# Kernel optimization log

Measured on AMD Instinct MI355X. Metric: run time of the kernel, lower is better.

## Reference

```python
import jax, jax.numpy as jnp
import numpy as np

N, E, G = 100000, 1600000, 64   # nodes, edges, graphs
IN, H, OUT = 32, 128, 3


def setup_inputs() -> dict:
    key = jax.random.key(0)
    ks = jax.random.split(key, 24)
    def w(k, i, o):
        return (jax.random.normal(k, (i, o), jnp.float32) / np.sqrt(i)).astype(jnp.float32)
    inp = {
        "x": jax.random.normal(ks[0], (N, IN), jnp.float32),
        "edge_index": jax.random.randint(ks[1], (2, E), 0, N, dtype=jnp.int32).astype(jnp.int64),
        "batch": jnp.sort(jax.random.randint(ks[2], (N,), 0, G, dtype=jnp.int32)).astype(jnp.int64),
        # SAGEConv layer 0 (in->hidden): lin_l (neighbors, with bias), lin_r (root, no bias)
        "Wl0": w(ks[3], IN, H), "bl0": jnp.zeros((H,), jnp.float32), "Wr0": w(ks[4], IN, H),
        # SAGEConv layers 1,2 (hidden->hidden)
        "Wl1": w(ks[5], H, H), "bl1": jnp.zeros((H,), jnp.float32), "Wr1": w(ks[6], H, H),
        "Wl2": w(ks[7], H, H), "bl2": jnp.zeros((H,), jnp.float32), "Wr2": w(ks[8], H, H),
        # output head
        "Wfc": w(ks[9], H, OUT), "bfc": jnp.zeros((OUT,), jnp.float32),
        # aux MLP on (dim1, dim3)
        "Wa1": w(ks[10], 2, H), "ba1": jnp.zeros((H,), jnp.float32),
        "Wa2": w(ks[11], H, H), "ba2": jnp.zeros((H,), jnp.float32),
        "Wao": w(ks[12], H, 1), "bao": jnp.zeros((1,), jnp.float32),
    }
    return inp


def _sage_conv(x, src, dst, Wl, bl, Wr):
    # PyG SAGEConv (mean aggr): out = lin_l(mean_{j in N(i)} x_j) + lin_r(x_i)
    msg = x[src]                                   # [E, d] gather
    agg = jax.ops.segment_sum(msg, dst, num_segments=N)
    cnt = jax.ops.segment_sum(jnp.ones((src.shape[0],), x.dtype), dst, num_segments=N)
    mean = agg / jnp.maximum(cnt, 1.0)[:, None]
    return mean @ Wl + bl + x @ Wr


def reference(x, edge_index, batch,
              Wl0, bl0, Wr0, Wl1, bl1, Wr1, Wl2, bl2, Wr2,
              Wfc, bfc, Wa1, ba1, Wa2, ba2, Wao, bao):
    src, dst = edge_index[0], edge_index[1]
    h = jax.nn.relu(_sage_conv(x, src, dst, Wl0, bl0, Wr0))   # dropout is identity in eval
    h = jax.nn.relu(_sage_conv(h, src, dst, Wl1, bl1, Wr1))
    h = jax.nn.relu(_sage_conv(h, src, dst, Wl2, bl2, Wr2))
    main = h @ Wfc + bfc                                      # [N, 3]
    dim1, dim3 = main[:, 0], main[:, 2]
    aux_in = jnp.stack([dim1, dim3], axis=-1)                 # [N, 2]
    a = jax.nn.relu(aux_in @ Wa1 + ba1)
    a = jax.nn.relu(a @ Wa2 + ba2)
    aux_out = (a @ Wao + bao)[:, 0]                           # [N]
    final = jnp.stack([dim1, aux_out, dim3], axis=-1)         # [N, 3]
    # global mean pool over graph ids
    s = jax.ops.segment_sum(final, batch, num_segments=G)
    c = jax.ops.segment_sum(jnp.ones((final.shape[0],), final.dtype), batch, num_segments=G)
    return s / jnp.maximum(c, 1.0)[:, None]                   # [G, 3]
```

## Files before the change

### kernel.cpp

```cpp
#include <hip/hip_runtime.h>

#define NR 128
#define PART_CH 4096
typedef unsigned short ushortT;
typedef __attribute__((ext_vector_type(8))) short short8;
typedef __attribute__((ext_vector_type(4))) float float4v;
typedef __attribute__((ext_vector_type(2))) float float2v;

__device__ __forceinline__ unsigned short f32_to_bf16_rne(float f) {
    unsigned u = __float_as_uint(f);
    unsigned r = (u + 0x7fffu + ((u >> 16) & 1u)) >> 16;
    return (unsigned short)r;
}

__device__ __forceinline__ unsigned char f32_to_fp8(float f) {
    return (unsigned char)(__builtin_amdgcn_cvt_pk_fp8_f32(f, f, 0, false) & 0xff);
}

__device__ __forceinline__ void accum8(float* acc, uint4 v) {
    unsigned u[4] = {v.x, v.y, v.z, v.w};
#pragma unroll
    for (int q = 0; q < 4; q++) {
        acc[2 * q]     += __uint_as_float(u[q] << 16);
        acc[2 * q + 1] += __uint_as_float(u[q] & 0xffff0000u);
    }
}

__device__ __forceinline__ void accum16_fp8(float* acc, uint4 v) {
    unsigned u[4] = {v.x, v.y, v.z, v.w};
#pragma unroll
    for (int q = 0; q < 4; q++) {
        float2v lo = __builtin_amdgcn_cvt_pk_f32_fp8(u[q], false);
        float2v hi = __builtin_amdgcn_cvt_pk_f32_fp8(u[q], true);
        acc[4 * q + 0] += lo.x;
        acc[4 * q + 1] += lo.y;
        acc[4 * q + 2] += hi.x;
        acc[4 * q + 3] += hi.y;
    }
}


__launch_bounds__(256)
__global__ void bucket_count(const int* __restrict__ dst, int* __restrict__ bcnt, int E, int NB) {
    __shared__ int h[1024];
    int t = threadIdx.x;
    for (int j = t; j < NB; j += 256) h[j] = 0;
    __syncthreads();
    int e0 = blockIdx.x * PART_CH;
    int e1 = min(e0 + PART_CH, E);
    for (int base = e0; base < e1; base += 2048) {
        int idx = base + t;
        int d[8];
        int cnt = 0;
#pragma unroll
        for (int u = 0; u < 8; u++) {
            int e = idx + u * 256;
            if (e < e1) d[cnt++] = dst[e];
        }
        for (int u = 0; u < cnt; u++) atomicAdd(&h[d[u] >> 7], 1);
    }
    __syncthreads();
    for (int j = t; j < NB; j += 256) {
        int v = h[j];
        if (v) atomicAdd(&bcnt[j], v);
    }
}

__launch_bounds__(256)
__global__ void bucket_scan(const int* __restrict__ bcnt, int* __restrict__ bstart,
                            int* __restrict__ gcur, int NB, int E) {
    __shared__ int sh[256];
    int t = threadIdx.x;
    int v[4];
    int tot = 0;
#pragma unroll
    for (int j = 0; j < 4; j++) {
        int idx = t * 4 + j;
        v[j] = (idx < NB) ? bcnt[idx] : 0;
        tot += v[j];
    }
    sh[t] = tot;
    __syncthreads();
    for (int off = 1; off < 256; off <<= 1) {
        int add = (t >= off) ? sh[t - off] : 0;
        __syncthreads();
        sh[t] += add;
        __syncthreads();
    }
    int run = sh[t] - tot;
#pragma unroll
    for (int j = 0; j < 4; j++) {
        int idx = t * 4 + j;
        if (idx < NB) { bstart[idx] = run; gcur[idx] = run; }
        run += v[j];
    }
    if (t == 0) bstart[NB] = E;
}

__launch_bounds__(256)
__global__ void partition_edges(const int* __restrict__ src, const int* __restrict__ dst,
                                int* __restrict__ gcur, unsigned* __restrict__ packed,
                                int E, int NB) {
    __shared__ int hist[1024];
    __shared__ int base[1024];
    int t = threadIdx.x;
    int e0 = blockIdx.x * PART_CH;
    int e1 = min(e0 + PART_CH, E);
    for (int j = t; j < NB; j += 256) hist[j] = 0;
    __syncthreads();
    for (int bb = e0; bb < e1; bb += 2048) {
        int idx = bb + t;
        int d[8];
        int cnt = 0;
#pragma unroll
        for (int u = 0; u < 8; u++) {
            int e = idx + u * 256;
            if (e < e1) d[cnt++] = dst[e];
        }
        for (int u = 0; u < cnt; u++) atomicAdd(&hist[d[u] >> 7], 1);
    }
    __syncthreads();
    for (int j = t; j < NB; j += 256) {
        int h = hist[j];
        base[j] = h ? atomicAdd(&gcur[j], h) : 0;
    }
    __syncthreads();
    for (int j = t; j < NB; j += 256) hist[j] = base[j];
    __syncthreads();
    for (int bb = e0; bb < e1; bb += 2048) {
        int idx = bb + t;
        int d[8], s[8];
        int cnt = 0;
#pragma unroll
        for (int u = 0; u < 8; u++) {
            int e = idx + u * 256;
            if (e < e1) { d[cnt] = dst[e]; s[cnt] = src[e]; cnt++; }
        }
        for (int u = 0; u < cnt; u++) {
            int dd = d[u];
            int pos = atomicAdd(&hist[dd >> 7], 1);
            packed[pos] = (unsigned)s[u] | ((unsigned)(dd & (NR - 1)) << 17);
        }
    }
}

__launch_bounds__(256)
__global__ void bucket_sort(const unsigned* __restrict__ packed, const int* __restrict__ bstart,
                            int* __restrict__ row_start, int* __restrict__ srcs, int N) {
    __shared__ int cnt[NR];
    __shared__ int sc[NR];
    __shared__ int cur[NR];
    int b = blockIdx.x, t = threadIdx.x;
    int nb0 = b * NR;
    int nnode = min(NR, N - nb0);
    int lo = bstart[b], hi = bstart[b + 1];
    if (t < NR) cnt[t] = 0;
    __syncthreads();
    for (int bb = lo; bb < hi; bb += 2048) {
        int idx = bb + t;
        unsigned pk[8];
        int c = 0;
#pragma unroll
        for (int u = 0; u < 8; u++) {
            int e = idx + u * 256;
            if (e < hi) pk[c++] = packed[e];
        }
        for (int u = 0; u < c; u++) atomicAdd(&cnt[pk[u] >> 17], 1);
    }
    __syncthreads();
    if (t < NR) sc[t] = cnt[t];
    __syncthreads();
    for (int off = 1; off < NR; off <<= 1) {
        int add = (t >= off && t < NR) ? sc[t - off] : 0;
        __syncthreads();
        if (t < NR) sc[t] += add;
        __syncthreads();
    }
    if (t < nnode) {
        int s = lo + sc[t] - cnt[t];
        row_start[nb0 + t] = s;
        cur[t] = s;
    }
    if (t == 0 && nb0 + nnode == N) row_start[N] = hi;
    __syncthreads();
    for (int bb = lo; bb < hi; bb += 2048) {
        int idx = bb + t;
        unsigned pk[8];
        int c = 0;
#pragma unroll
        for (int u = 0; u < 8; u++) {
            int e = idx + u * 256;
            if (e < hi) pk[c++] = packed[e];
        }
        for (int u = 0; u < c; u++) {
            int pos = atomicAdd(&cur[pk[u] >> 17], 1);
            srcs[pos] = (int)(pk[u] & 0x1FFFFu);
        }
    }
}


__global__ void prep_fused(const float* __restrict__ x, ushortT* __restrict__ xbf, int n4,
                           const float* __restrict__ Wl0, const float* __restrict__ Wr0,
                           const float* __restrict__ Wl1, const float* __restrict__ Wr1,
                           const float* __restrict__ Wl2, const float* __restrict__ Wr2,
                           const float* __restrict__ Wa2,
                           ushortT* __restrict__ Wt0, ushortT* __restrict__ Wt1,
                           ushortT* __restrict__ Wt2, ushortT* __restrict__ Wa2t) {
    int tid0 = blockIdx.x * 256 + threadIdx.x;
    if (tid0 < n4) {
        float4 v = ((const float4*)x)[tid0];
        ushort4 o;
        o.x = f32_to_bf16_rne(v.x);
        o.y = f32_to_bf16_rne(v.y);
        o.z = f32_to_bf16_rne(v.z);
        o.w = f32_to_bf16_rne(v.w);
        ((ushort4*)xbf)[tid0] = o;
        return;
    }
    int tid = tid0 - n4;
    if (tid < 8192) {
        int col = tid >> 6, k = tid & 63;
        float v = (k < 32) ? Wl0[k * 128 + col] : Wr0[(k - 32) * 128 + col];
        Wt0[col * 64 + ((k + 8 * col) & 63)] = f32_to_bf16_rne(v);
    } else if (tid < 8192 + 32768) {
        int j = tid - 8192;
        int col = j >> 8, k = j & 255;
        float v = (k < 128) ? Wl1[k * 128 + col] : Wr1[(k - 128) * 128 + col];
        Wt1[col * 256 + ((k + 8 * col) & 255)] = f32_to_bf16_rne(v);
    } else if (tid < 8192 + 65536) {
        int j = tid - 8192 - 32768;
        int col = j >> 8, k = j & 255;
        float v = (k < 128) ? Wl2[k * 128 + col] : Wr2[(k - 128) * 128 + col];
        Wt2[col * 256 + ((k + 8 * col) & 255)] = f32_to_bf16_rne(v);
    } else if (tid < 8192 + 65536 + 16384) {
        int j = tid - 8192 - 65536;
        int col = j >> 7, k = j & 127;
        Wa2t[col * 128 + ((k + 8 * col) & 127)] = f32_to_bf16_rne(Wa2[k * 128 + col]);
    }
}


template <int CPN>
__launch_bounds__(256)
__global__ void aggregate_mean_bf16(const uint4* __restrict__ hin, ushortT* __restrict__ out,
                                    const int* __restrict__ srcs, const int* __restrict__ rs, int n) {
    constexpr int TPN = CPN / 2;
    int tid = blockIdx.x * 256 + threadIdx.x;
    if (tid >= n * TPN) return;
    int i = tid / TPN;
    int c = tid & (TPN - 1);
    int lo = rs[i], hi = rs[i + 1];
    float acc0[8], acc1[8];
#pragma unroll
    for (int q = 0; q < 8; q++) { acc0[q] = 0.f; acc1[q] = 0.f; }
    int e = lo;
    for (; e + 8 <= hi; e += 8) {
        int s[8];
#pragma unroll
        for (int u = 0; u < 8; u++) s[u] = srcs[e + u];
        uint4 va[8], vb[8];
#pragma unroll
        for (int u = 0; u < 8; u++) {
            va[u] = hin[(size_t)s[u] * CPN + c];
            vb[u] = hin[(size_t)s[u] * CPN + c + TPN];
        }
#pragma unroll
        for (int u = 0; u < 8; u++) { accum8(acc0, va[u]); accum8(acc1, vb[u]); }
    }
    for (; e < hi; ++e) {
        int s = srcs[e];
        accum8(acc0, hin[(size_t)s * CPN + c]);
        accum8(acc1, hin[(size_t)s * CPN + c + TPN]);
    }
    float inv = 1.0f / (float)max(hi - lo, 1);
    uint4 o0, o1;
    o0.x = (unsigned)f32_to_bf16_rne(acc0[0] * inv) | ((unsigned)f32_to_bf16_rne(acc0[1] * inv) << 16);
    o0.y = (unsigned)f32_to_bf16_rne(acc0[2] * inv) | ((unsigned)f32_to_bf16_rne(acc0[3] * inv) << 16);
    o0.z = (unsigned)f32_to_bf16_rne(acc0[4] * inv) | ((unsigned)f32_to_bf16_rne(acc0[5] * inv) << 16);
    o0.w = (unsigned)f32_to_bf16_rne(acc0[6] * inv) | ((unsigned)f32_to_bf16_rne(acc0[7] * inv) << 16);
    o1.x = (unsigned)f32_to_bf16_rne(acc1[0] * inv) | ((unsigned)f32_to_bf16_rne(acc1[1] * inv) << 16);
    o1.y = (unsigned)f32_to_bf16_rne(acc1[2] * inv) | ((unsigned)f32_to_bf16_rne(acc1[3] * inv) << 16);
    o1.z = (unsigned)f32_to_bf16_rne(acc1[4] * inv) | ((unsigned)f32_to_bf16_rne(acc1[5] * inv) << 16);
    o1.w = (unsigned)f32_to_bf16_rne(acc1[6] * inv) | ((unsigned)f32_to_bf16_rne(acc1[7] * inv) << 16);
    ((uint4*)out)[(size_t)i * CPN + c] = o0;
    ((uint4*)out)[(size_t)i * CPN + c + TPN] = o1;
}


__launch_bounds__(256)
__global__ void aggregate_mean_fp8(const uint4* __restrict__ hin, ushortT* __restrict__ out,
                                   const int* __restrict__ srcs, const int* __restrict__ rs, int n) {
    int tid = blockIdx.x * 256 + threadIdx.x;
    if (tid >= n * 8) return;
    int i = tid >> 3;
    int c = tid & 7;
    int lo = rs[i], hi = rs[i + 1];
    float acc[16];
#pragma unroll
    for (int q = 0; q < 16; q++) acc[q] = 0.f;
    int e = lo;
    for (; e + 8 <= hi; e += 8) {
        int s[8];
#pragma unroll
        for (int u = 0; u < 8; u++) s[u] = srcs[e + u];
        uint4 v[8];
#pragma unroll
        for (int u = 0; u < 8; u++) v[u] = hin[(size_t)s[u] * 8 + c];
#pragma unroll
        for (int u = 0; u < 8; u++) accum16_fp8(acc, v[u]);
    }
    for (; e + 4 <= hi; e += 4) {
        int s[4];
#pragma unroll
        for (int u = 0; u < 4; u++) s[u] = srcs[e + u];
        uint4 v[4];
#pragma unroll
        for (int u = 0; u < 4; u++) v[u] = hin[(size_t)s[u] * 8 + c];
#pragma unroll
        for (int u = 0; u < 4; u++) accum16_fp8(acc, v[u]);
    }
    for (; e < hi; ++e) accum16_fp8(acc, hin[(size_t)srcs[e] * 8 + c]);
    float inv = 1.0f / (float)max(hi - lo, 1);
    uint4 o0, o1;
    o0.x = (unsigned)f32_to_bf16_rne(acc[0] * inv)  | ((unsigned)f32_to_bf16_rne(acc[1] * inv) << 16);
    o0.y = (unsigned)f32_to_bf16_rne(acc[2] * inv)  | ((unsigned)f32_to_bf16_rne(acc[3] * inv) << 16);
    o0.z = (unsigned)f32_to_bf16_rne(acc[4] * inv)  | ((unsigned)f32_to_bf16_rne(acc[5] * inv) << 16);
    o0.w = (unsigned)f32_to_bf16_rne(acc[6] * inv)  | ((unsigned)f32_to_bf16_rne(acc[7] * inv) << 16);
    o1.x = (unsigned)f32_to_bf16_rne(acc[8] * inv)  | ((unsigned)f32_to_bf16_rne(acc[9] * inv) << 16);
    o1.y = (unsigned)f32_to_bf16_rne(acc[10] * inv) | ((unsigned)f32_to_bf16_rne(acc[11] * inv) << 16);
    o1.z = (unsigned)f32_to_bf16_rne(acc[12] * inv) | ((unsigned)f32_to_bf16_rne(acc[13] * inv) << 16);
    o1.w = (unsigned)f32_to_bf16_rne(acc[14] * inv) | ((unsigned)f32_to_bf16_rne(acc[15] * inv) << 16);
    ((uint4*)out)[(size_t)i * 16 + c * 2]     = o0;
    ((uint4*)out)[(size_t)i * 16 + c * 2 + 1] = o1;
}


template <int KH, bool OUT_BF16, bool OUT_FP8>
__launch_bounds__(256, 2)
__global__ void gemm_mfma(const ushortT* __restrict__ Am, const ushortT* __restrict__ Ah,
                          const ushortT* __restrict__ Wt, const float* __restrict__ bias,
                          float* __restrict__ outf, ushortT* __restrict__ outbf,
                          unsigned char* __restrict__ outf8, int n) {
    constexpr int KT = 2 * KH;
    __shared__ ushortT sW[128 * KT];
    int t = threadIdx.x;
    constexpr int TOT16 = 128 * KT * 2 / 16;
    {
        const uint4* Wg = (const uint4*)Wt;
        uint4* Ws = (uint4*)sW;
        for (int j = t; j < TOT16; j += 256) Ws[j] = Wg[j];
    }
    __syncthreads();
    int wv = t >> 6, lane = t & 63;
    int q = lane >> 4, cid = lane & 15;
    int rbase = blockIdx.x * 128 + wv * 32;
    int r0 = rbase + cid, r1 = r0 + 16;
    int r0c = min(r0, n - 1), r1c = min(r1, n - 1);
    float4v acc[2][8];
#pragma unroll
    for (int i = 0; i < 2; i++)
#pragma unroll
        for (int j = 0; j < 8; j++) acc[i][j] = (float4v){0.f, 0.f, 0.f, 0.f};
    int swz = q * 8 + 8 * cid;
#pragma unroll
    for (int ks = 0; ks < KT / 32; ++ks) {
        int kk = ks * 32;
        const ushortT* abase = (kk < KH) ? Am : Ah;
        int kc = (kk < KH) ? kk : kk - KH;
        short8 a0 = *(const short8*)(abase + (size_t)r0c * KH + kc + q * 8);
        short8 a1 = *(const short8*)(abase + (size_t)r1c * KH + kc + q * 8);
#pragma unroll
        for (int j = 0; j < 8; ++j) {
            int col = j * 16 + cid;
            int p = (kk + swz + j * 128) & (KT - 1);
            short8 b = *(const short8*)(sW + col * KT + p);
            acc[0][j] = __builtin_amdgcn_mfma_f32_16x16x32_bf16(a0, b, acc[0][j], 0, 0, 0);
            acc[1][j] = __builtin_amdgcn_mfma_f32_16x16x32_bf16(a1, b, acc[1][j], 0, 0, 0);
        }
    }
    float bo[8];
#pragma unroll
    for (int j = 0; j < 8; ++j) bo[j] = bias[j * 16 + cid];
#pragma unroll
    for (int i = 0; i < 2; ++i) {
#pragma unroll
        for (int rr = 0; rr < 4; ++rr) {
            int row = rbase + i * 16 + q * 4 + rr;
            if (row < n) {
#pragma unroll
                for (int j = 0; j < 8; ++j) {
                    int col = j * 16 + cid;
                    float v = fmaxf(acc[i][j][rr] + bo[j], 0.f);
                    if (OUT_BF16) outbf[(size_t)row * 128 + col] = f32_to_bf16_rne(v);
                    if (OUT_FP8)  outf8[(size_t)row * 128 + col] = f32_to_fp8(v);
                    if (!OUT_BF16 && !OUT_FP8) outf[(size_t)row * 128 + col] = v;
                }
            }
        }
    }
}


template <int KH>
__launch_bounds__(256, 2)
__global__ void gemm_mfma_fin(const ushortT* __restrict__ Am, const ushortT* __restrict__ Ah,
                              const ushortT* __restrict__ Wt, const float* __restrict__ bias,
                              const float* __restrict__ Wfc, const float* __restrict__ bfc,
                              float* __restrict__ fin, int n) {
    constexpr int KT = 2 * KH;
    __shared__ ushortT sW[128 * KT];
    int t = threadIdx.x;
    constexpr int TOT16 = 128 * KT * 2 / 16;
    {
        const uint4* Wg = (const uint4*)Wt;
        uint4* Ws = (uint4*)sW;
        for (int j = t; j < TOT16; j += 256) Ws[j] = Wg[j];
    }
    __syncthreads();
    int wv = t >> 6, lane = t & 63;
    int q = lane >> 4, cid = lane & 15;
    int rbase = blockIdx.x * 128 + wv * 32;
    int r0 = rbase + cid, r1 = r0 + 16;
    int r0c = min(r0, n - 1), r1c = min(r1, n - 1);
    float4v acc[2][8];
#pragma unroll
    for (int i = 0; i < 2; i++)
#pragma unroll
        for (int j = 0; j < 8; j++) acc[i][j] = (float4v){0.f, 0.f, 0.f, 0.f};
    int swz = q * 8 + 8 * cid;
#pragma unroll
    for (int ks = 0; ks < KT / 32; ++ks) {
        int kk = ks * 32;
        const ushortT* abase = (kk < KH) ? Am : Ah;
        int kc = (kk < KH) ? kk : kk - KH;
        short8 a0 = *(const short8*)(abase + (size_t)r0c * KH + kc + q * 8);
        short8 a1 = *(const short8*)(abase + (size_t)r1c * KH + kc + q * 8);
#pragma unroll
        for (int j = 0; j < 8; ++j) {
            int col = j * 16 + cid;
            int p = (kk + swz + j * 128) & (KT - 1);
            short8 b = *(const short8*)(sW + col * KT + p);
            acc[0][j] = __builtin_amdgcn_mfma_f32_16x16x32_bf16(a0, b, acc[0][j], 0, 0, 0);
            acc[1][j] = __builtin_amdgcn_mfma_f32_16x16x32_bf16(a1, b, acc[1][j], 0, 0, 0);
        }
    }
    float bo[8], w1[8], w3[8];
#pragma unroll
    for (int j = 0; j < 8; ++j) {
        int col = j * 16 + cid;
        bo[j] = bias[col];
        w1[j] = Wfc[col * 3 + 0];
        w3[j] = Wfc[col * 3 + 2];
    }
    float bfc0 = bfc[0], bfc2 = bfc[2];
#pragma unroll
    for (int i = 0; i < 2; ++i) {
#pragma unroll
        for (int rr = 0; rr < 4; ++rr) {
            float p1 = 0.f, p3 = 0.f;
#pragma unroll
            for (int j = 0; j < 8; ++j) {
                float v = fmaxf(acc[i][j][rr] + bo[j], 0.f);
                p1 += v * w1[j];
                p3 += v * w3[j];
            }
            p1 += __shfl_xor(p1, 1, 64); p3 += __shfl_xor(p3, 1, 64);
            p1 += __shfl_xor(p1, 2, 64); p3 += __shfl_xor(p3, 2, 64);
            p1 += __shfl_xor(p1, 4, 64); p3 += __shfl_xor(p3, 4, 64);
            p1 += __shfl_xor(p1, 8, 64); p3 += __shfl_xor(p3, 8, 64);
            int row = rbase + i * 16 + q * 4 + rr;
            if (cid == 0 && row < n) {
                fin[(size_t)row * 3 + 0] = p1 + bfc0;
                fin[(size_t)row * 3 + 2] = p3 + bfc2;
            }
        }
    }
}


__launch_bounds__(256, 4)
__global__ void head_mfma(const ushortT* __restrict__ Wa2t, const float* __restrict__ Wa1,
                          const float* __restrict__ ba1, const float* __restrict__ ba2,
                          const float* __restrict__ Wao, const float* __restrict__ bao,
                          float* __restrict__ fin, int n) {
    __shared__ ushortT sW[128 * 128];
    __shared__ float sD1[128], sD3[128];
    __shared__ float sWa1a[128], sWa1b[128], sBa1[128];
    int t = threadIdx.x;
    {
        const uint4* Wg = (const uint4*)Wa2t;
        uint4* Ws = (uint4*)sW;
        for (int j = t; j < 2048; j += 256) Ws[j] = Wg[j];
    }
    int rbase = blockIdx.x * 128;
    if (t < 128) {
        sWa1a[t] = Wa1[t];
        sWa1b[t] = Wa1[128 + t];
        sBa1[t] = ba1[t];
        int row = min(rbase + t, n - 1);
        sD1[t] = fin[(size_t)row * 3 + 0];
        sD3[t] = fin[(size_t)row * 3 + 2];
    }
    __syncthreads();
    int wv = t >> 6, lane = t & 63;
    int q = lane >> 4, cid = lane & 15;
    int rl0 = wv * 32 + cid, rl1 = rl0 + 16;
    float d1a = sD1[rl0], d3a = sD3[rl0];
    float d1b = sD1[rl1], d3b = sD3[rl1];
    float4v acc[2][8];
#pragma unroll
    for (int i = 0; i < 2; i++)
#pragma unroll
        for (int j = 0; j < 8; j++) acc[i][j] = (float4v){0.f, 0.f, 0.f, 0.f};
    int swz = q * 8 + 8 * cid;
#pragma unroll
    for (int ks = 0; ks < 4; ++ks) {
        int k0 = ks * 32 + q * 8;
        short8 a0, a1;
#pragma unroll
        for (int j = 0; j < 8; ++j) {
            int k = k0 + j;
            float w0 = sWa1a[k], w1 = sWa1b[k], bb = sBa1[k];
            float v0 = fmaxf(fmaf(d1a, w0, fmaf(d3a, w1, bb)), 0.f);
            float v1 = fmaxf(fmaf(d1b, w0, fmaf(d3b, w1, bb)), 0.f);
            a0[j] = (short)f32_to_bf16_rne(v0);
            a1[j] = (short)f32_to_bf16_rne(v1);
        }
        int p = (ks * 32 + swz) & 127;
#pragma unroll
        for (int j = 0; j < 8; ++j) {
            short8 b = *(const short8*)(sW + (j * 16 + cid) * 128 + p);
            acc[0][j] = __builtin_amdgcn_mfma_f32_16x16x32_bf16(a0, b, acc[0][j], 0, 0, 0);
            acc[1][j] = __builtin_amdgcn_mfma_f32_16x16x32_bf16(a1, b, acc[1][j], 0, 0, 0);
        }
    }
    float b2[8], wo[8];
#pragma unroll
    for (int j = 0; j < 8; ++j) {
        int col = j * 16 + cid;
        b2[j] = ba2[col];
        wo[j] = Wao[col];
    }
    float bao0 = bao[0];
#pragma unroll
    for (int i = 0; i < 2; ++i) {
#pragma unroll
        for (int rr = 0; rr < 4; ++rr) {
            float s = 0.f;
#pragma unroll
            for (int j = 0; j < 8; ++j) s += fmaxf(acc[i][j][rr] + b2[j], 0.f) * wo[j];
            s += __shfl_xor(s, 1, 64);
            s += __shfl_xor(s, 2, 64);
            s += __shfl_xor(s, 4, 64);
            s += __shfl_xor(s, 8, 64);
            int row = rbase + wv * 32 + i * 16 + q * 4 + rr;
            if (cid == 0 && row < n) fin[(size_t)row * 3 + 1] = s + bao0;
        }
    }
}


__global__ void pool_kernel(const float* __restrict__ fin, const int* __restrict__ batch,
                            float* __restrict__ out, int n) {
    int g = blockIdx.x, t = threadIdx.x;
    int lo = 0, hi = n;
    while (lo < hi) { int mid = (lo + hi) >> 1; if (batch[mid] < g) lo = mid + 1; else hi = mid; }
    int start = lo;
    lo = 0; hi = n;
    while (lo < hi) { int mid = (lo + hi) >> 1; if (batch[mid] < g + 1) lo = mid + 1; else hi = mid; }
    int end = lo;
    float s0 = 0.f, s1 = 0.f, s2 = 0.f;
    for (int i = start + t; i < end; i += 256) {
        s0 += fin[(size_t)i * 3 + 0];
        s1 += fin[(size_t)i * 3 + 1];
        s2 += fin[(size_t)i * 3 + 2];
    }
    __shared__ float r0[256], r1[256], r2[256];
    r0[t] = s0; r1[t] = s1; r2[t] = s2;
    __syncthreads();
    for (int off = 128; off > 0; off >>= 1) {
        if (t < off) { r0[t] += r0[t + off]; r1[t] += r1[t + off]; r2[t] += r2[t + off]; }
        __syncthreads();
    }
    if (t == 0) {
        float c = (float)max(end - start, 1);
        out[g * 3 + 0] = r0[0] / c;
        out[g * 3 + 1] = r1[0] / c;
        out[g * 3 + 2] = r2[0] / c;
    }
}


extern "C" void kernel_launch(void* const* d_in, const int* in_sizes, int n_in,
                              void* d_out, int out_size, void* d_ws, size_t ws_size,
                              hipStream_t stream) {
    const float* x    = (const float*)d_in[0];
    const int*   ei   = (const int*)d_in[1];
    const int*   batch= (const int*)d_in[2];
    const float* Wl0  = (const float*)d_in[3];
    const float* bl0  = (const float*)d_in[4];
    const float* Wr0  = (const float*)d_in[5];
    const float* Wl1  = (const float*)d_in[6];
    const float* bl1  = (const float*)d_in[7];
    const float* Wr1  = (const float*)d_in[8];
    const float* Wl2  = (const float*)d_in[9];
    const float* bl2  = (const float*)d_in[10];
    const float* Wr2  = (const float*)d_in[11];
    const float* Wfc  = (const float*)d_in[12];
    const float* bfc  = (const float*)d_in[13];
    const float* Wa1  = (const float*)d_in[14];
    const float* ba1  = (const float*)d_in[15];
    const float* Wa2  = (const float*)d_in[16];
    const float* ba2  = (const float*)d_in[17];
    const float* Wao  = (const float*)d_in[18];
    const float* bao  = (const float*)d_in[19];

    const int N = in_sizes[0] / 32;
    const int E = in_sizes[1] / 2;
    const int G = out_size / 3;
    const int* src = ei;
    const int* dst = ei + E;
    float* out = (float*)d_out;
    const int NB = (N + NR - 1) / NR;

    char* p = (char*)d_ws;
    auto carve = [&](size_t bytes) {
        void* r = (void*)p;
        p += (bytes + 255) & ~(size_t)255;
        return r;
    };
    int*           bcnt     = (int*)carve((size_t)NB * 4);
    int*           bstart   = (int*)carve((size_t)(NB + 1) * 4);
    int*           gcur     = (int*)carve((size_t)NB * 4);
    int*           row_start= (int*)carve((size_t)(N + 1) * 4);
    unsigned*      packed   = (unsigned*)carve((size_t)E * 4);
    int*           srcs     = (int*)carve((size_t)E * 4);
    ushortT*       aggbf    = (ushortT*)carve((size_t)N * 128 * 2);
    ushortT*       xbf      = (ushortT*)carve((size_t)N * 32 * 2);
    ushortT*       hbf0     = (ushortT*)carve((size_t)N * 128 * 2);
    ushortT*       hbf1     = (ushortT*)carve((size_t)N * 128 * 2);
    unsigned char* hf8_0    = (unsigned char*)carve((size_t)N * 128);
    unsigned char* hf8_1    = (unsigned char*)carve((size_t)N * 128);
    float*         fin      = (float*)carve((size_t)N * 3 * 4);
    ushortT*       Wt0      = (ushortT*)carve((size_t)128 * 64 * 2);
    ushortT*       Wt1      = (ushortT*)carve((size_t)128 * 256 * 2);
    ushortT*       Wt2      = (ushortT*)carve((size_t)128 * 256 * 2);
    ushortT*       Wa2t     = (ushortT*)carve((size_t)128 * 128 * 2);

    const int gemm_grid = (N + 127) / 128;
    const int part_grid = (E + PART_CH - 1) / PART_CH;
    const int n4 = N * 32 / 4;

    prep_fused<<<(n4 + 90112 + 255) / 256, 256, 0, stream>>>(
        x, xbf, n4, Wl0, Wr0, Wl1, Wr1, Wl2, Wr2, Wa2, Wt0, Wt1, Wt2, Wa2t);

    hipMemsetAsync(bcnt, 0, (size_t)NB * 4, stream);
    bucket_count<<<part_grid, 256, 0, stream>>>(dst, bcnt, E, NB);
    bucket_scan<<<1, 256, 0, stream>>>(bcnt, bstart, gcur, NB, E);
    partition_edges<<<part_grid, 256, 0, stream>>>(src, dst, gcur, packed, E, NB);
    bucket_sort<<<NB, 256, 0, stream>>>(packed, bstart, row_start, srcs, N);

    aggregate_mean_bf16<4><<<(N * 2 + 255) / 256, 256, 0, stream>>>(
        (const uint4*)xbf, aggbf, srcs, row_start, N);
    gemm_mfma<32, true, true><<<gemm_grid, 256, 0, stream>>>(
        aggbf, xbf, Wt0, bl0, (float*)nullptr, hbf0, hf8_0, N);
    aggregate_mean_fp8<<<(N * 8 + 255) / 256, 256, 0, stream>>>(
        (const uint4*)hf8_0, aggbf, srcs, row_start, N);
    gemm_mfma<128, true, true><<<gemm_grid, 256, 0, stream>>>(
        aggbf, hbf0, Wt1, bl1, (float*)nullptr, hbf1, hf8_1, N);
    aggregate_mean_fp8<<<(N * 8 + 255) / 256, 256, 0, stream>>>(
        (const uint4*)hf8_1, aggbf, srcs, row_start, N);
    gemm_mfma_fin<128><<<gemm_grid, 256, 0, stream>>>(
        aggbf, hbf1, Wt2, bl2, Wfc, bfc, fin, N);

    head_mfma<<<gemm_grid, 256, 0, stream>>>(
        Wa2t, Wa1, ba1, ba2, Wao, bao, fin, N);

    pool_kernel<<<G, 256, 0, stream>>>(fin, batch, out, N);
}
```

Measured before the change: 364.4 us.

## Fuse neighbor mean aggregation into MFMA GEMM kernels and merge head into final layer

Each SAGE layer's gather-and-mean aggregation is now done inside the GEMM kernel. The aggregated rows are built directly in registers in the MFMA A-operand layout, which removes the aggbf intermediate write and read and three separate aggregate launches. The aux head MLP is folded into the final layer kernel, reusing shared memory, so a fin round-trip and a launch go away. In exchange, the GEMM blocks now carry the irregular gather latency with only 128 rows per block and 2 blocks per SM, so they get less memory-level parallelism than the old aggregation kernels, which used one thread per node slice.

```diff
diff --git a/kernel.cpp b/kernel.cpp
--- a/kernel.cpp
+++ b/kernel.cpp
@@ -23,19 +23,6 @@
     for (int q = 0; q < 4; q++) {
         acc[2 * q]     += __uint_as_float(u[q] << 16);
         acc[2 * q + 1] += __uint_as_float(u[q] & 0xffff0000u);
-    }
-}
-
-__device__ __forceinline__ void accum16_fp8(float* acc, uint4 v) {
-    unsigned u[4] = {v.x, v.y, v.z, v.w};
-#pragma unroll
-    for (int q = 0; q < 4; q++) {
-        float2v lo = __builtin_amdgcn_cvt_pk_f32_fp8(u[q], false);
-        float2v hi = __builtin_amdgcn_cvt_pk_f32_fp8(u[q], true);
-        acc[4 * q + 0] += lo.x;
-        acc[4 * q + 1] += lo.y;
-        acc[4 * q + 2] += hi.x;
-        acc[4 * q + 3] += hi.y;
     }
 }
 
@@ -241,122 +228,85 @@
 }
 
 
-template <int CPN>
-__launch_bounds__(256)
-__global__ void aggregate_mean_bf16(const uint4* __restrict__ hin, ushortT* __restrict__ out,
-                                    const int* __restrict__ srcs, const int* __restrict__ rs, int n) {
-    constexpr int TPN = CPN / 2;
-    int tid = blockIdx.x * 256 + threadIdx.x;
-    if (tid >= n * TPN) return;
-    int i = tid / TPN;
-    int c = tid & (TPN - 1);
-    int lo = rs[i], hi = rs[i + 1];
-    float acc0[8], acc1[8];
-#pragma unroll
-    for (int q = 0; q < 8; q++) { acc0[q] = 0.f; acc1[q] = 0.f; }
-    int e = lo;
-    for (; e + 8 <= hi; e += 8) {
-        int s[8];
-#pragma unroll
-        for (int u = 0; u < 8; u++) s[u] = srcs[e + u];
-        uint4 va[8], vb[8];
-#pragma unroll
-        for (int u = 0; u < 8; u++) {
-            va[u] = hin[(size_t)s[u] * CPN + c];
-            vb[u] = hin[(size_t)s[u] * CPN + c + TPN];
-        }
-#pragma unroll
-        for (int u = 0; u < 8; u++) { accum8(acc0, va[u]); accum8(acc1, vb[u]); }
-    }
-    for (; e < hi; ++e) {
-        int s = srcs[e];
-        accum8(acc0, hin[(size_t)s * CPN + c]);
-        accum8(acc1, hin[(size_t)s * CPN + c + TPN]);
-    }
-    float inv = 1.0f / (float)max(hi - lo, 1);
-    uint4 o0, o1;
-    o0.x = (unsigned)f32_to_bf16_rne(acc0[0] * inv) | ((unsigned)f32_to_bf16_rne(acc0[1] * inv) << 16);
-    o0.y = (unsigned)f32_to_bf16_rne(acc0[2] * inv) | ((unsigned)f32_to_bf16_rne(acc0[3] * inv) << 16);
-    o0.z = (unsigned)f32_to_bf16_rne(acc0[4] * inv) | ((unsigned)f32_to_bf16_rne(acc0[5] * inv) << 16);
-    o0.w = (unsigned)f32_to_bf16_rne(acc0[6] * inv) | ((unsigned)f32_to_bf16_rne(acc0[7] * inv) << 16);
-    o1.x = (unsigned)f32_to_bf16_rne(acc1[0] * inv) | ((unsigned)f32_to_bf16_rne(acc1[1] * inv) << 16);
-    o1.y = (unsigned)f32_to_bf16_rne(acc1[2] * inv) | ((unsigned)f32_to_bf16_rne(acc1[3] * inv) << 16);
-    o1.z = (unsigned)f32_to_bf16_rne(acc1[4] * inv) | ((unsigned)f32_to_bf16_rne(acc1[5] * inv) << 16);
-    o1.w = (unsigned)f32_to_bf16_rne(acc1[6] * inv) | ((unsigned)f32_to_bf16_rne(acc1[7] * inv) << 16);
-    ((uint4*)out)[(size_t)i * CPN + c] = o0;
-    ((uint4*)out)[(size_t)i * CPN + c + TPN] = o1;
-}
-
-
-__launch_bounds__(256)
-__global__ void aggregate_mean_fp8(const uint4* __restrict__ hin, ushortT* __restrict__ out,
-                                   const int* __restrict__ srcs, const int* __restrict__ rs, int n) {
-    int tid = blockIdx.x * 256 + threadIdx.x;
-    if (tid >= n * 8) return;
-    int i = tid >> 3;
-    int c = tid & 7;
-    int lo = rs[i], hi = rs[i + 1];
-    float acc[16];
-#pragma unroll
-    for (int q = 0; q < 16; q++) acc[q] = 0.f;
-    int e = lo;
-    for (; e + 8 <= hi; e += 8) {
-        int s[8];
-#pragma unroll
-        for (int u = 0; u < 8; u++) s[u] = srcs[e + u];
-        uint4 v[8];
-#pragma unroll
-        for (int u = 0; u < 8; u++) v[u] = hin[(size_t)s[u] * 8 + c];
-#pragma unroll
-        for (int u = 0; u < 8; u++) accum16_fp8(acc, v[u]);
-    }
-    for (; e + 4 <= hi; e += 4) {
-        int s[4];
-#pragma unroll
-        for (int u = 0; u < 4; u++) s[u] = srcs[e + u];
-        uint4 v[4];
-#pragma unroll
-        for (int u = 0; u < 4; u++) v[u] = hin[(size_t)s[u] * 8 + c];
-#pragma unroll
-        for (int u = 0; u < 4; u++) accum16_fp8(acc, v[u]);
-    }
-    for (; e < hi; ++e) accum16_fp8(acc, hin[(size_t)srcs[e] * 8 + c]);
-    float inv = 1.0f / (float)max(hi - lo, 1);
-    uint4 o0, o1;
-    o0.x = (unsigned)f32_to_bf16_rne(acc[0] * inv)  | ((unsigned)f32_to_bf16_rne(acc[1] * inv) << 16);
-    o0.y = (unsigned)f32_to_bf16_rne(acc[2] * inv)  | ((unsigned)f32_to_bf16_rne(acc[3] * inv) << 16);
-    o0.z = (unsigned)f32_to_bf16_rne(acc[4] * inv)  | ((unsigned)f32_to_bf16_rne(acc[5] * inv) << 16);
-    o0.w = (unsigned)f32_to_bf16_rne(acc[6] * inv)  | ((unsigned)f32_to_bf16_rne(acc[7] * inv) << 16);
-    o1.x = (unsigned)f32_to_bf16_rne(acc[8] * inv)  | ((unsigned)f32_to_bf16_rne(acc[9] * inv) << 16);
-    o1.y = (unsigned)f32_to_bf16_rne(acc[10] * inv) | ((unsigned)f32_to_bf16_rne(acc[11] * inv) << 16);
-    o1.z = (unsigned)f32_to_bf16_rne(acc[12] * inv) | ((unsigned)f32_to_bf16_rne(acc[13] * inv) << 16);
-    o1.w = (unsigned)f32_to_bf16_rne(acc[14] * inv) | ((unsigned)f32_to_bf16_rne(acc[15] * inv) << 16);
-    ((uint4*)out)[(size_t)i * 16 + c * 2]     = o0;
-    ((uint4*)out)[(size_t)i * 16 + c * 2 + 1] = o1;
-}
-
-
-template <int KH, bool OUT_BF16, bool OUT_FP8>
+template <bool FP8, int NKS>
+__device__ __forceinline__ void gather_accum(const void* __restrict__ gat, int s, int q, float* ag) {
+    if constexpr (FP8) {
+        const uint2* hp = (const uint2*)gat;
+        size_t base = (size_t)s * 16 + q;
+        uint2 c[NKS];
+#pragma unroll
+        for (int ks = 0; ks < NKS; ks++) c[ks] = hp[base + ks * 4];
+#pragma unroll
+        for (int ks = 0; ks < NKS; ks++) {
+            float2v l0 = __builtin_amdgcn_cvt_pk_f32_fp8(c[ks].x, false);
+            float2v h0 = __builtin_amdgcn_cvt_pk_f32_fp8(c[ks].x, true);
+            float2v l1 = __builtin_amdgcn_cvt_pk_f32_fp8(c[ks].y, false);
+            float2v h1 = __builtin_amdgcn_cvt_pk_f32_fp8(c[ks].y, true);
+            ag[ks * 8 + 0] += l0.x; ag[ks * 8 + 1] += l0.y;
+            ag[ks * 8 + 2] += h0.x; ag[ks * 8 + 3] += h0.y;
+            ag[ks * 8 + 4] += l1.x; ag[ks * 8 + 5] += l1.y;
+            ag[ks * 8 + 6] += h1.x; ag[ks * 8 + 7] += h1.y;
+        }
+    } else {
+        const uint4* xp = (const uint4*)gat;
+        uint4 v = xp[(size_t)s * 4 + q];
+        accum8(ag, v);
+    }
+}
+
+template <int KH, bool IN_FP8>
 __launch_bounds__(256, 2)
-__global__ void gemm_mfma(const ushortT* __restrict__ Am, const ushortT* __restrict__ Ah,
-                          const ushortT* __restrict__ Wt, const float* __restrict__ bias,
-                          float* __restrict__ outf, ushortT* __restrict__ outbf,
-                          unsigned char* __restrict__ outf8, int n) {
+__global__ void gemm_agg(const void* __restrict__ gat, const ushortT* __restrict__ Ah,
+                         const int* __restrict__ srcs, const int* __restrict__ rs,
+                         const ushortT* __restrict__ Wt, const float* __restrict__ bias,
+                         ushortT* __restrict__ outbf, unsigned char* __restrict__ outf8, int n) {
     constexpr int KT = 2 * KH;
-    __shared__ ushortT sW[128 * KT];
+    constexpr int NKS = KH / 32;
+    __shared__ __attribute__((aligned(16))) ushortT sW[128 * KT];
     int t = threadIdx.x;
     constexpr int TOT16 = 128 * KT * 2 / 16;
     {
         const uint4* Wg = (const uint4*)Wt;
         uint4* Ws = (uint4*)sW;
-        for (int j = t; j < TOT16; j += 256) Ws[j] = Wg[j];
-    }
-    __syncthreads();
+#pragma unroll
+        for (int j = 0; j < TOT16 / 256; j++) Ws[t + j * 256] = Wg[t + j * 256];
+    }
     int wv = t >> 6, lane = t & 63;
     int q = lane >> 4, cid = lane & 15;
     int rbase = blockIdx.x * 128 + wv * 32;
     int r0 = rbase + cid, r1 = r0 + 16;
     int r0c = min(r0, n - 1), r1c = min(r1, n - 1);
+
+    float ag0[NKS * 8], ag1[NKS * 8];
+#pragma unroll
+    for (int j = 0; j < NKS * 8; j++) { ag0[j] = 0.f; ag1[j] = 0.f; }
+    int lo0 = rs[r0c], n0 = rs[r0c + 1] - lo0;
+    int lo1 = rs[r1c], n1 = rs[r1c + 1] - lo1;
+    int mx = max(n0, n1);
+    for (int i = 0; i < mx; i += 2) {
+        bool v00 = i < n0, v01 = (i + 1) < n0;
+        bool v10 = i < n1, v11 = (i + 1) < n1;
+        int s00 = srcs[v00 ? lo0 + i : 0];
+        int s01 = srcs[v01 ? lo0 + i + 1 : 0];
+        int s10 = srcs[v10 ? lo1 + i : 0];
+        int s11 = srcs[v11 ? lo1 + i + 1 : 0];
+        if (v00) gather_accum<IN_FP8, NKS>(gat, s00, q, ag0);
+        if (v01) gather_accum<IN_FP8, NKS>(gat, s01, q, ag0);
+        if (v10) gather_accum<IN_FP8, NKS>(gat, s10, q, ag1);
+        if (v11) gather_accum<IN_FP8, NKS>(gat, s11, q, ag1);
+    }
+    float inv0 = 1.0f / (float)max(n0, 1);
+    float inv1 = 1.0f / (float)max(n1, 1);
+    short8 am0[NKS], am1[NKS];
+#pragma unroll
+    for (int ks = 0; ks < NKS; ks++)
+#pragma unroll
+        for (int j = 0; j < 8; j++) {
+            am0[ks][j] = (short)f32_to_bf16_rne(ag0[ks * 8 + j] * inv0);
+            am1[ks][j] = (short)f32_to_bf16_rne(ag1[ks * 8 + j] * inv1);
+        }
+    __syncthreads();
+
     float4v acc[2][8];
 #pragma unroll
     for (int i = 0; i < 2; i++)
@@ -366,10 +316,15 @@
 #pragma unroll
     for (int ks = 0; ks < KT / 32; ++ks) {
         int kk = ks * 32;
-        const ushortT* abase = (kk < KH) ? Am : Ah;
-        int kc = (kk < KH) ? kk : kk - KH;
-        short8 a0 = *(const short8*)(abase + (size_t)r0c * KH + kc + q * 8);
-        short8 a1 = *(const short8*)(abase + (size_t)r1c * KH + kc + q * 8);
+        short8 a0, a1;
+        if (ks < NKS) {
+            a0 = am0[ks];
+            a1 = am1[ks];
+        } else {
+            int kc = kk - KH;
+            a0 = *(const short8*)(Ah + (size_t)r0c * KH + kc + q * 8);
+            a1 = *(const short8*)(Ah + (size_t)r1c * KH + kc + q * 8);
+        }
 #pragma unroll
         for (int j = 0; j < 8; ++j) {
             int col = j * 16 + cid;
@@ -392,9 +347,8 @@
                 for (int j = 0; j < 8; ++j) {
                     int col = j * 16 + cid;
                     float v = fmaxf(acc[i][j][rr] + bo[j], 0.f);
-                    if (OUT_BF16) outbf[(size_t)row * 128 + col] = f32_to_bf16_rne(v);
-                    if (OUT_FP8)  outf8[(size_t)row * 128 + col] = f32_to_fp8(v);
-                    if (!OUT_BF16 && !OUT_FP8) outf[(size_t)row * 128 + col] = v;
+                    outbf[(size_t)row * 128 + col] = f32_to_bf16_rne(v);
+                    outf8[(size_t)row * 128 + col] = f32_to_fp8(v);
                 }
             }
         }
@@ -402,27 +356,64 @@
 }
 
 
-template <int KH>
 __launch_bounds__(256, 2)
-__global__ void gemm_mfma_fin(const ushortT* __restrict__ Am, const ushortT* __restrict__ Ah,
-                              const ushortT* __restrict__ Wt, const float* __restrict__ bias,
-                              const float* __restrict__ Wfc, const float* __restrict__ bfc,
-                              float* __restrict__ fin, int n) {
-    constexpr int KT = 2 * KH;
-    __shared__ ushortT sW[128 * KT];
+__global__ void gemm_agg_fin(const void* __restrict__ gat, const ushortT* __restrict__ Ah,
+                             const int* __restrict__ srcs, const int* __restrict__ rs,
+                             const ushortT* __restrict__ Wt, const float* __restrict__ bias,
+                             const float* __restrict__ Wfc, const float* __restrict__ bfc,
+                             const ushortT* __restrict__ Wa2t, const float* __restrict__ Wa1,
+                             const float* __restrict__ ba1, const float* __restrict__ ba2,
+                             const float* __restrict__ Wao, const float* __restrict__ bao,
+                             float* __restrict__ fin, int n) {
+    constexpr int KH = 128, KT = 256, NKS = 4;
+    __shared__ __attribute__((aligned(16))) ushortT sW[128 * KT];
+    __shared__ float sD1[128], sD3[128];
+    __shared__ float sWa1a[128], sWa1b[128], sBa1[128];
     int t = threadIdx.x;
-    constexpr int TOT16 = 128 * KT * 2 / 16;
     {
         const uint4* Wg = (const uint4*)Wt;
         uint4* Ws = (uint4*)sW;
-        for (int j = t; j < TOT16; j += 256) Ws[j] = Wg[j];
-    }
-    __syncthreads();
+#pragma unroll
+        for (int j = 0; j < 16; j++) Ws[t + j * 256] = Wg[t + j * 256];
+    }
+    if (t < 128) { sWa1a[t] = Wa1[t]; sWa1b[t] = Wa1[128 + t]; sBa1[t] = ba1[t]; }
     int wv = t >> 6, lane = t & 63;
     int q = lane >> 4, cid = lane & 15;
-    int rbase = blockIdx.x * 128 + wv * 32;
+    int blk0 = blockIdx.x * 128;
+    int rbase = blk0 + wv * 32;
     int r0 = rbase + cid, r1 = r0 + 16;
     int r0c = min(r0, n - 1), r1c = min(r1, n - 1);
+
+    float ag0[NKS * 8], ag1[NKS * 8];
+#pragma unroll
+    for (int j = 0; j < NKS * 8; j++) { ag0[j] = 0.f; ag1[j] = 0.f; }
+    int lo0 = rs[r0c], n0 = rs[r0c + 1] - lo0;
+    int lo1 = rs[r1c], n1 = rs[r1c + 1] - lo1;
+    int mx = max(n0, n1);
+    for (int i = 0; i < mx; i += 2) {
+        bool v00 = i < n0, v01 = (i + 1) < n0;
+        bool v10 = i < n1, v11 = (i + 1) < n1;
+        int s00 = srcs[v00 ? lo0 + i : 0];
+        int s01 = srcs[v01 ? lo0 + i + 1 : 0];
+        int s10 = srcs[v10 ? lo1 + i : 0];
+        int s11 = srcs[v11 ? lo1 + i + 1 : 0];
+        if (v00) gather_accum<true, NKS>(gat, s00, q, ag0);
+        if (v01) gather_accum<true, NKS>(gat, s01, q, ag0);
+        if (v10) gather_accum<true, NKS>(gat, s10, q, ag1);
+        if (v11) gather_accum<true, NKS>(gat, s11, q, ag1);
+    }
+    float inv0 = 1.0f / (float)max(n0, 1);
+    float inv1 = 1.0f / (float)max(n1, 1);
+    short8 am0[NKS], am1[NKS];
+#pragma unroll
+    for (int ks = 0; ks < NKS; ks++)
+#pragma unroll
+        for (int j = 0; j < 8; j++) {
+            am0[ks][j] = (short)f32_to_bf16_rne(ag0[ks * 8 + j] * inv0);
+            am1[ks][j] = (short)f32_to_bf16_rne(ag1[ks * 8 + j] * inv1);
+        }
+    __syncthreads();
+
     float4v acc[2][8];
 #pragma unroll
     for (int i = 0; i < 2; i++)
@@ -432,10 +423,15 @@
 #pragma unroll
     for (int ks = 0; ks < KT / 32; ++ks) {
         int kk = ks * 32;
-        const ushortT* abase = (kk < KH) ? Am : Ah;
-        int kc = (kk < KH) ? kk : kk - KH;
-        short8 a0 = *(const short8*)(abase + (size_t)r0c * KH + kc + q * 8);
-        short8 a1 = *(const short8*)(abase + (size_t)r1c * KH + kc + q * 8);
+        short8 a0, a1;
+        if (ks < NKS) {
+            a0 = am0[ks];
+            a1 = am1[ks];
+        } else {
+            int kc = kk - KH;
+            a0 = *(const short8*)(Ah + (size_t)r0c * KH + kc + q * 8);
+            a1 = *(const short8*)(Ah + (size_t)r1c * KH + kc + q * 8);
+        }
 #pragma unroll
         for (int j = 0; j < 8; ++j) {
             int col = j * 16 + cid;
@@ -445,6 +441,7 @@
             acc[1][j] = __builtin_amdgcn_mfma_f32_16x16x32_bf16(a1, b, acc[1][j], 0, 0, 0);
         }
     }
+
     float bo[8], w1[8], w3[8];
 #pragma unroll
     for (int j = 0; j < 8; ++j) {
@@ -469,51 +466,37 @@
             p1 += __shfl_xor(p1, 2, 64); p3 += __shfl_xor(p3, 2, 64);
             p1 += __shfl_xor(p1, 4, 64); p3 += __shfl_xor(p3, 4, 64);
             p1 += __shfl_xor(p1, 8, 64); p3 += __shfl_xor(p3, 8, 64);
-            int row = rbase + i * 16 + q * 4 + rr;
-            if (cid == 0 && row < n) {
-                fin[(size_t)row * 3 + 0] = p1 + bfc0;
-                fin[(size_t)row * 3 + 2] = p3 + bfc2;
+            int rowl = wv * 32 + i * 16 + q * 4 + rr;
+            if (cid == 0) {
+                float d1 = p1 + bfc0, d3 = p3 + bfc2;
+                sD1[rowl] = d1;
+                sD3[rowl] = d3;
+                int row = blk0 + rowl;
+                if (row < n) {
+                    fin[(size_t)row * 3 + 0] = d1;
+                    fin[(size_t)row * 3 + 2] = d3;
+                }
             }
         }
     }
-}
-
-
-__launch_bounds__(256, 4)
-__global__ void head_mfma(const ushortT* __restrict__ Wa2t, const float* __restrict__ Wa1,
-                          const float* __restrict__ ba1, const float* __restrict__ ba2,
-                          const float* __restrict__ Wao, const float* __restrict__ bao,
-                          float* __restrict__ fin, int n) {
-    __shared__ ushortT sW[128 * 128];
-    __shared__ float sD1[128], sD3[128];
-    __shared__ float sWa1a[128], sWa1b[128], sBa1[128];
-    int t = threadIdx.x;
+    __syncthreads();
+
     {
         const uint4* Wg = (const uint4*)Wa2t;
         uint4* Ws = (uint4*)sW;
-        for (int j = t; j < 2048; j += 256) Ws[j] = Wg[j];
-    }
-    int rbase = blockIdx.x * 128;
-    if (t < 128) {
-        sWa1a[t] = Wa1[t];
-        sWa1b[t] = Wa1[128 + t];
-        sBa1[t] = ba1[t];
-        int row = min(rbase + t, n - 1);
-        sD1[t] = fin[(size_t)row * 3 + 0];
-        sD3[t] = fin[(size_t)row * 3 + 2];
-    }
-    __syncthreads();
-    int wv = t >> 6, lane = t & 63;
-    int q = lane >> 4, cid = lane & 15;
+#pragma unroll
+        for (int j = 0; j < 8; j++) Ws[t + j * 256] = Wg[t + j * 256];
+    }
+    __syncthreads();
+
     int rl0 = wv * 32 + cid, rl1 = rl0 + 16;
     float d1a = sD1[rl0], d3a = sD3[rl0];
     float d1b = sD1[rl1], d3b = sD3[rl1];
-    float4v acc[2][8];
+    float4v hacc[2][8];
 #pragma unroll
     for (int i = 0; i < 2; i++)
 #pragma unroll
-        for (int j = 0; j < 8; j++) acc[i][j] = (float4v){0.f, 0.f, 0.f, 0.f};
-    int swz = q * 8 + 8 * cid;
+        for (int j = 0; j < 8; j++) hacc[i][j] = (float4v){0.f, 0.f, 0.f, 0.f};
 #pragma unroll
     for (int ks = 0; ks < 4; ++ks) {
         int k0 = ks * 32 + q * 8;
@@ -521,9 +504,9 @@
 #pragma unroll
         for (int j = 0; j < 8; ++j) {
             int k = k0 + j;
-            float w0 = sWa1a[k], w1 = sWa1b[k], bb = sBa1[k];
-            float v0 = fmaxf(fmaf(d1a, w0, fmaf(d3a, w1, bb)), 0.f);
-            float v1 = fmaxf(fmaf(d1b, w0, fmaf(d3b, w1, bb)), 0.f);
+            float w0 = sWa1a[k], w1h = sWa1b[k], bb = sBa1[k];
+            float v0 = fmaxf(fmaf(d1a, w0, fmaf(d3a, w1h, bb)), 0.f);
+            float v1 = fmaxf(fmaf(d1b, w0, fmaf(d3b, w1h, bb)), 0.f);
             a0[j] = (short)f32_to_bf16_rne(v0);
             a1[j] = (short)f32_to_bf16_rne(v1);
         }
@@ -531,8 +514,8 @@
 #pragma unroll
         for (int j = 0; j < 8; ++j) {
             short8 b = *(const short8*)(sW + (j * 16 + cid) * 128 + p);
-            acc[0][j] = __builtin_amdgcn_mfma_f32_16x16x32_bf16(a0, b, acc[0][j], 0, 0, 0);
-            acc[1][j] = __builtin_amdgcn_mfma_f32_16x16x32_bf16(a1, b, acc[1][j], 0, 0, 0);
+            hacc[0][j] = __builtin_amdgcn_mfma_f32_16x16x32_bf16(a0, b, hacc[0][j], 0, 0, 0);
+            hacc[1][j] = __builtin_amdgcn_mfma_f32_16x16x32_bf16(a1, b, hacc[1][j], 0, 0, 0);
         }
     }
     float b2[8], wo[8];
@@ -549,12 +532,12 @@
         for (int rr = 0; rr < 4; ++rr) {
             float s = 0.f;
 #pragma unroll
-            for (int j = 0; j < 8; ++j) s += fmaxf(acc[i][j][rr] + b2[j], 0.f) * wo[j];
+            for (int j = 0; j < 8; ++j) s += fmaxf(hacc[i][j][rr] + b2[j], 0.f) * wo[j];
             s += __shfl_xor(s, 1, 64);
             s += __shfl_xor(s, 2, 64);
             s += __shfl_xor(s, 4, 64);
             s += __shfl_xor(s, 8, 64);
-            int row = rbase + wv * 32 + i * 16 + q * 4 + rr;
+            int row = blk0 + wv * 32 + i * 16 + q * 4 + rr;
             if (cid == 0 && row < n) fin[(size_t)row * 3 + 1] = s + bao0;
         }
     }
@@ -636,7 +619,6 @@
     int*           row_start= (int*)carve((size_t)(N + 1) * 4);
     unsigned*      packed   = (unsigned*)carve((size_t)E * 4);
     int*           srcs     = (int*)carve((size_t)E * 4);
-    ushortT*       aggbf    = (ushortT*)carve((size_t)N * 128 * 2);
     ushortT*       xbf      = (ushortT*)carve((size_t)N * 32 * 2);
     ushortT*       hbf0     = (ushortT*)carve((size_t)N * 128 * 2);
     ushortT*       hbf1     = (ushortT*)carve((size_t)N * 128 * 2);
@@ -661,20 +643,12 @@
     partition_edges<<<part_grid, 256, 0, stream>>>(src, dst, gcur, packed, E, NB);
     bucket_sort<<<NB, 256, 0, stream>>>(packed, bstart, row_start, srcs, N);
 
-    aggregate_mean_bf16<4><<<(N * 2 + 255) / 256, 256, 0, stream>>>(
-        (const uint4*)xbf, aggbf, srcs, row_start, N);
-    gemm_mfma<32, true, true><<<gemm_grid, 256, 0, stream>>>(
-        aggbf, xbf, Wt0, bl0, (float*)nullptr, hbf0, hf8_0, N);
-    aggregate_mean_fp8<<<(N * 8 + 255) / 256, 256, 0, stream>>>(
-        (const uint4*)hf8_0, aggbf, srcs, row_start, N);
-    gemm_mfma<128, true, true><<<gemm_grid, 256, 0, stream>>>(
-        aggbf, hbf0, Wt1, bl1, (float*)nullptr, hbf1, hf8_1, N);
-    aggregate_mean_fp8<<<(N * 8 + 255) / 256, 256, 0, stream>>>(
-        (const uint4*)hf8_1, aggbf, srcs, row_start, N);
-    gemm_mfma_fin<128><<<gemm_grid, 256, 0, stream>>>(
-        aggbf, hbf1, Wt2, bl2, Wfc, bfc, fin, N);
-
-    head_mfma<<<gemm_grid, 256, 0, stream>>>(
+    gemm_agg<32, false><<<gemm_grid, 256, 0, stream>>>(
+        (const void*)xbf, xbf, srcs, row_start, Wt0, bl0, hbf0, hf8_0, N);
+    gemm_agg<128, true><<<gemm_grid, 256, 0, stream>>>(
+        (const void*)hf8_0, hbf0, srcs, row_start, Wt1, bl1, hbf1, hf8_1, N);
+    gemm_agg_fin<<<gemm_grid, 256, 0, stream>>>(
+        (const void*)hf8_1, hbf1, srcs, row_start, Wt2, bl2, Wfc, bfc,
         Wa2t, Wa1, ba1, ba2, Wao, bao, fin, N);
 
     pool_kernel<<<G, 256, 0, stream>>>(fin, batch, out, N);
```

Measured after the change: 408.9 us. 1.12x slower.
